# Performance work log

Hardware: AMD Instinct MI355X
Metric: run time of the kernel (lower is better)

Reference implementation:

```python
import jax, jax.numpy as jnp
import numpy as np

DIM = 2048
HEADS = 32
DIM_HEAD = 64
FF_INNER = DIM * 4
SCALE_BASE = 512
FUSED = HEADS * DIM_HEAD + DIM_HEAD + DIM_HEAD + FF_INNER * 2  # 18560


def setup_inputs() -> dict:
    key = jax.random.key(0)
    k1, k2, k3, k4 = jax.random.split(key, 4)
    b, n = 2, 2048
    x = jax.random.normal(k1, (b, n, DIM), dtype=jnp.float32)
    W_fused = jax.random.normal(k2, (FUSED, DIM), dtype=jnp.float32) * 0.02
    W_attn_out = jax.random.normal(k3, (DIM, HEADS * DIM_HEAD), dtype=jnp.float32) * 0.02
    W_ff_out = jax.random.normal(k4, (DIM, FF_INNER), dtype=jnp.float32) * 0.02
    gamma = jnp.ones((DIM,), dtype=jnp.float32)
    return {"x": x, "gamma": gamma, "W_fused": W_fused,
            "W_attn_out": W_attn_out, "W_ff_out": W_ff_out}


def _rotate_half(t):
    t1, t2 = jnp.split(t, 2, axis=-1)
    return jnp.concatenate((-t2, t1), axis=-1)


def _rotary(n, dtype):
    # xpos rotary embeddings: freqs [n, dim_head], scale [n, dim_head]
    inv_freq = 1.0 / (10000.0 ** (jnp.arange(0, DIM_HEAD, 2, dtype=jnp.float32) / DIM_HEAD))
    t = jnp.arange(n, dtype=jnp.float32)
    freqs = t[:, None] * inv_freq[None, :]
    freqs = jnp.concatenate((freqs, freqs), axis=-1)
    power = (t - n // 2) / SCALE_BASE
    scale_base_vec = (jnp.arange(0, DIM_HEAD, 2, dtype=jnp.float32) + 0.4 * DIM_HEAD) / (1.4 * DIM_HEAD)
    scale = scale_base_vec[None, :] ** power[:, None]
    scale = jnp.concatenate((scale, scale), axis=-1)
    return freqs.astype(dtype), scale.astype(dtype)


def _apply_rotary(pos, t, scale):
    return t * jnp.cos(pos) * scale + _rotate_half(t) * jnp.sin(pos) * scale


def reference(x, gamma, W_fused, W_attn_out, W_ff_out):
    b, n, d = x.shape
    # LayerNorm (beta fixed at zero)
    mu = jnp.mean(x, axis=-1, keepdims=True)
    var = jnp.mean((x - mu) ** 2, axis=-1, keepdims=True)
    xn = (x - mu) * jax.lax.rsqrt(var + 1e-5) * gamma

    # fused QKV + FF projection
    proj = jnp.einsum('bnd,fd->bnf', xn, W_fused)
    attn_inner = HEADS * DIM_HEAD
    q = proj[..., :attn_inner]
    k = proj[..., attn_inner:attn_inner + DIM_HEAD]
    v = proj[..., attn_inner + DIM_HEAD:attn_inner + 2 * DIM_HEAD]
    ff = proj[..., attn_inner + 2 * DIM_HEAD:]

    # multi-query attention with xpos rotary
    q = q.reshape(b, n, HEADS, DIM_HEAD).transpose(0, 2, 1, 3)  # b h n d
    q = q * (DIM_HEAD ** -0.5)
    pos, scale = _rotary(n, x.dtype)
    q = _apply_rotary(pos, q, scale)          # broadcasts over b,h
    k = _apply_rotary(pos, k, 1.0 / scale)    # k is [b, n, dim_head]

    sim = jnp.einsum('bhid,bjd->bhij', q, k)
    causal_mask = jnp.triu(jnp.ones((n, n), dtype=bool), k=1)
    sim = jnp.where(causal_mask, -jnp.finfo(sim.dtype).max, sim)
    attn = jax.nn.softmax(sim, axis=-1)
    out = jnp.einsum('bhij,bjd->bhid', attn, v)
    out = out.transpose(0, 2, 1, 3).reshape(b, n, attn_inner)
    attn_out = jnp.einsum('bnf,df->bnd', out, W_attn_out)

    # SwiGLU FF
    ff_x, gate = jnp.split(ff, 2, axis=-1)
    ff_hidden = jax.nn.silu(gate) * ff_x
    ff_out = jnp.einsum('bnf,df->bnd', ff_hidden, W_ff_out)

    return attn_out + ff_out
```

## Files before the change

### kernel.cpp

```cpp
#include <hip/hip_runtime.h>
#include <cstdint>
#include <cstddef>

typedef __bf16 bf16;
typedef float f32x4 __attribute__((ext_vector_type(4)));
typedef bf16  bf16x4 __attribute__((ext_vector_type(4)));
typedef bf16  bf16x8 __attribute__((ext_vector_type(8)));

#define DIMD   2048
#define HEADS  32
#define DH     64
#define FFI    8192
#define FUSEDN 18560
#define FUSEDP 18688
#define BB     2
#define NN     2048
#define MROWS  4096
#define K2     10240

__device__ __forceinline__ void gl_lds16(const void* g, void* l) {
  __builtin_amdgcn_global_load_lds(
      (__attribute__((address_space(1))) void*)const_cast<void*>(g),
      (__attribute__((address_space(3))) void*)l, 16, 0, 0);
}

template <int THREADS>
__device__ __forceinline__ void stage_i(const bf16* g, long ldk,
                                        bf16* region, int instr, int tid) {
  int row = instr * (THREADS / 8) + (tid >> 3);
  int cs  = (tid & 7) ^ (row & 7);
  gl_lds16(g + (size_t)row * ldk + cs * 8,
           region + (size_t)instr * (THREADS * 8) + (size_t)(tid & ~63) * 8);
}

struct SrcT { const bf16* g; long ldk; };

template <typename FA, typename FB>
__device__ __forceinline__ void gemm_2ph(FA fa, FB fb, const int NT,
    bf16* As, bf16* Bs, f32x4 (&acc)[4][4],
    const int tid, const int wrow, const int nbase, const int l15, const int h4)
{
  const char* aP[2]; const char* bP[2];
  const int arow = wrow + l15, brow = nbase + l15;
#pragma unroll
  for (int ks = 0; ks < 2; ks++) {
    aP[ks] = (const char*)As + arow * 128 + (((ks * 4 + h4) ^ (arow & 7)) * 16);
    bP[ks] = (const char*)Bs + brow * 128 + (((ks * 4 + h4) ^ (brow & 7)) * 16);
  }
  for (int t = 0; t < NT; ++t) {
    __syncthreads();
    {
      auto a = fa(t); auto b = fb(t);
#pragma unroll
      for (int q = 0; q < 4; q++) stage_i<256>(a.g, a.ldk, As, q, tid);
#pragma unroll
      for (int q = 0; q < 4; q++) stage_i<256>(b.g, b.ldk, Bs, q, tid);
    }
    __syncthreads();
#pragma unroll
    for (int ks = 0; ks < 2; ks++) {
      bf16x8 af[4], bfr[4];
#pragma unroll
      for (int m_ = 0; m_ < 4; m_++) af[m_]  = *(const bf16x8*)(aP[ks] + m_ * 2048);
#pragma unroll
      for (int n_ = 0; n_ < 4; n_++) bfr[n_] = *(const bf16x8*)(bP[ks] + n_ * 2048);
#pragma unroll
      for (int m_ = 0; m_ < 4; m_++)
#pragma unroll
        for (int n_ = 0; n_ < 4; n_++)
          acc[m_][n_] = __builtin_amdgcn_mfma_f32_16x16x32_bf16(af[m_], bfr[n_], acc[m_][n_], 0, 0, 0);
    }
  }
}

__global__ void k_cvt_perm(const float* __restrict__ s, bf16* __restrict__ d, long total8) {
  long stride = (long)gridDim.x * blockDim.x;
  for (long i = (long)blockIdx.x * blockDim.x + threadIdx.x; i < total8; i += stride) {
    long e = i << 3;
    int p = (int)(e >> 11);
    int c = (int)(e & 2047);
    int orig;
    if (p < 2176) orig = p;
    else {
      int q = p - 2176, g = q >> 6, o = q & 63;
      orig = (o < 32) ? (2176 + g * 32 + o) : (2176 + 8192 + g * 32 + (o - 32));
    }
    const float* src = s + (size_t)orig * 2048 + c;
    float4 v0 = *(const float4*)src;
    float4 v1 = *(const float4*)(src + 4);
    bf16x8 o8;
    o8[0]=(bf16)v0.x; o8[1]=(bf16)v0.y; o8[2]=(bf16)v0.z; o8[3]=(bf16)v0.w;
    o8[4]=(bf16)v1.x; o8[5]=(bf16)v1.y; o8[6]=(bf16)v1.z; o8[7]=(bf16)v1.w;
    *(bf16x8*)(d + e) = o8;
  }
}

__global__ void k_cvt_str8(const float* __restrict__ s, bf16* __restrict__ d,
                           long total8, int colshift, int dstride, int doff) {
  long stride = (long)gridDim.x * blockDim.x;
  for (long i = (long)blockIdx.x * blockDim.x + threadIdx.x; i < total8; i += stride) {
    long e = i << 3;
    long r = e >> colshift;
    int  c = (int)(e & ((1L << colshift) - 1));
    float4 v0 = *(const float4*)(s + e);
    float4 v1 = *(const float4*)(s + e + 4);
    bf16x8 o;
    o[0]=(bf16)v0.x; o[1]=(bf16)v0.y; o[2]=(bf16)v0.z; o[3]=(bf16)v0.w;
    o[4]=(bf16)v1.x; o[5]=(bf16)v1.y; o[6]=(bf16)v1.z; o[7]=(bf16)v1.w;
    *(bf16x8*)(d + r * (long)dstride + doff + c) = o;
  }
}

__global__ __launch_bounds__(256) void k_ln(const float* __restrict__ x,
                                            const float* __restrict__ g,
                                            bf16* __restrict__ xn) {
  int row = blockIdx.x, t = threadIdx.x;
  const float4* xr = (const float4*)(x + (size_t)row * DIMD);
  float4 a = xr[t*2], b = xr[t*2+1];
  float s  = a.x+a.y+a.z+a.w + b.x+b.y+b.z+b.w;
  float s2 = a.x*a.x+a.y*a.y+a.z*a.z+a.w*a.w + b.x*b.x+b.y*b.y+b.z*b.z+b.w*b.w;
  for (int o = 1; o < 64; o <<= 1) { s += __shfl_xor(s, o); s2 += __shfl_xor(s2, o); }
  __shared__ float rs[8];
  if ((t & 63) == 0) { rs[t>>6] = s; rs[4 + (t>>6)] = s2; }
  __syncthreads();
  s = rs[0]+rs[1]+rs[2]+rs[3]; s2 = rs[4]+rs[5]+rs[6]+rs[7];
  float mu = s * (1.f/DIMD);
  float var = s2 * (1.f/DIMD) - mu*mu;
  float rstd = rsqrtf(var + 1e-5f);
  const float4* gr = (const float4*)g;
  float4 g0 = gr[t*2], g1 = gr[t*2+1];
  bf16x8 o;
  o[0]=(bf16)((a.x-mu)*rstd*g0.x); o[1]=(bf16)((a.y-mu)*rstd*g0.y);
  o[2]=(bf16)((a.z-mu)*rstd*g0.z); o[3]=(bf16)((a.w-mu)*rstd*g0.w);
  o[4]=(bf16)((b.x-mu)*rstd*g1.x); o[5]=(bf16)((b.y-mu)*rstd*g1.y);
  o[6]=(bf16)((b.z-mu)*rstd*g1.z); o[7]=(bf16)((b.w-mu)*rstd*g1.w);
  *(bf16x8*)(xn + (size_t)row * DIMD + t*8) = o;
}

__global__ __launch_bounds__(256, 3) void k_gemm1(const bf16* __restrict__ xn,
                                                  const bf16* __restrict__ wf,
                                                  bf16* __restrict__ q_raw,
                                                  bf16* __restrict__ k_buf,
                                                  bf16* __restrict__ v_t,
                                                  bf16* __restrict__ ffh) {
  __shared__ bf16 As[128*64];
  __shared__ bf16 Bs[128*64];
  const int tid = threadIdx.x, w = tid >> 6, l = tid & 63;
  const int l15 = l & 15, h4 = l >> 4;
  const int wrow = (w >> 1) * 64, nbase = (w & 1) * 64;
  const int bid = blockIdx.x;
  const int bs = (bid & 7) * 584 + (bid >> 3);
  const int mt = bs / 146, nt = bs - mt * 146;
  const int m0 = mt * 128, f0 = nt * 128;

  f32x4 acc[4][4];
#pragma unroll
  for (int i = 0; i < 4; i++)
#pragma unroll
    for (int j = 0; j < 4; j++) acc[i][j] = (f32x4){0.f,0.f,0.f,0.f};

  auto fa = [&](int t) -> SrcT { return SrcT{ xn + (size_t)m0 * DIMD + t * 64, (long)DIMD }; };
  auto fb = [&](int t) -> SrcT { return SrcT{ wf + (size_t)f0 * DIMD + t * 64, (long)DIMD }; };
  gemm_2ph(fa, fb, DIMD / 64, As, Bs, acc, tid, wrow, nbase, l15, h4);

  if (nt < 17) {
#pragma unroll
    for (int m_ = 0; m_ < 4; m_++)
#pragma unroll
      for (int nf = 0; nf < 4; nf++) {
        int fcol = f0 + nbase + nf*16 + l15;
#pragma unroll
        for (int j = 0; j < 4; j++) {
          int m = m0 + wrow + m_*16 + h4*4 + j;
          bf16 bv = (bf16)acc[m_][nf][j];
          int b = m >> 11, n = m & 2047;
          if (fcol < 2048) {
            int hh = fcol >> 6, d = fcol & 63;
            q_raw[(((size_t)(b*HEADS + hh) * NN + n) << 6) + d] = bv;
          } else if (fcol < 2112) {
            k_buf[(((size_t)(b*NN + n)) << 6) + (fcol - 2048)] = bv;
          } else if (fcol < 2176) {
            v_t[(((size_t)(b*DH + (fcol - 2112))) << 11) + n] = bv;
          }
        }
      }
  } else {
    int base = f0 + nbase;
    if (base < FUSEDN) {
      int g = (base - 2176) >> 6;
#pragma unroll
      for (int m_ = 0; m_ < 4; m_++)
#pragma unroll
        for (int nf = 0; nf < 2; nf++) {
          int xc = g*32 + nf*16 + l15;
#pragma unroll
          for (int j = 0; j < 4; j++) {
            int m = m0 + wrow + m_*16 + h4*4 + j;
            float xv = acc[m_][nf][j];
            float gv = acc[m_][nf+2][j];
            float sv = gv * (1.f / (1.f + __expf(-gv)));
            ffh[((size_t)m << 13) + xc] = (bf16)(sv * xv);
          }
        }
    }
  }
}

__global__ __launch_bounds__(256, 3) void k_gemm2(const bf16* __restrict__ u_o,
                                                  const bf16* __restrict__ ffh,
                                                  const bf16* __restrict__ wcat,
                                                  float* __restrict__ out,
                                                  float* __restrict__ part) {
  __shared__ bf16 As[128*64];
  __shared__ bf16 Bs[128*64];
  const int tid = threadIdx.x, w = tid >> 6, l = tid & 63;
  const int l15 = l & 15, h4 = l >> 4;
  const int wrow = (w >> 1) * 64, nbase = (w & 1) * 64;
  const int bid = blockIdx.x;
  const int kk = bid >> 9;
  const int inner = bid & 511;
  const int bs = (inner & 7) * 64 + (inner >> 3);
  const int mt = bs >> 4, nt = bs & 15;
  const int m0 = mt * 128, f0 = nt * 128;
  const int T0 = kk * 80;

  f32x4 acc[4][4];
#pragma unroll
  for (int i = 0; i < 4; i++)
#pragma unroll
    for (int j = 0; j < 4; j++) acc[i][j] = (f32x4){0.f,0.f,0.f,0.f};

  auto fa = [&](int t) -> SrcT {
    int tt = t + T0;
    if (tt < 32) return SrcT{ u_o + (size_t)m0 * DIMD + tt * 64, (long)DIMD };
    return SrcT{ ffh + (size_t)m0 * FFI + (tt - 32) * 64, (long)FFI };
  };
  auto fb = [&](int t) -> SrcT { return SrcT{ wcat + (size_t)f0 * K2 + (t + T0) * 64, (long)K2 }; };
  gemm_2ph(fa, fb, 80, As, Bs, acc, tid, wrow, nbase, l15, h4);

  float* dst = kk ? part : out;
#pragma unroll
  for (int m_ = 0; m_ < 4; m_++)
#pragma unroll
    for (int nf = 0; nf < 4; nf++) {
      int fcol = f0 + nbase + nf*16 + l15;
#pragma unroll
      for (int j = 0; j < 4; j++) {
        int m = m0 + wrow + m_*16 + h4*4 + j;
        dst[(size_t)m * DIMD + fcol] = acc[m_][nf][j];
      }
    }
}

__global__ void k_addout(float* __restrict__ out, const float* __restrict__ part, long total4) {
  long stride = (long)gridDim.x * blockDim.x;
  for (long i = (long)blockIdx.x * blockDim.x + threadIdx.x; i < total4; i += stride) {
    long e = i << 2;
    float4 a = *(const float4*)(out + e);
    float4 b = *(const float4*)(part + e);
    float4 r; r.x = a.x + b.x; r.y = a.y + b.y; r.z = a.z + b.z; r.w = a.w + b.w;
    *(float4*)(out + e) = r;
  }
}

__global__ void k_rope(bf16* __restrict__ q_raw, bf16* __restrict__ k_buf) {
  const long QT = (long)BB*HEADS*NN*32;
  const long TOT = QT + (long)BB*NN*32;
  long gid = (long)blockIdx.x * blockDim.x + threadIdx.x;
  if (gid >= TOT) return;
  bool isq = gid < QT;
  long idx = isq ? gid : gid - QT;
  int  i = (int)(idx & 31);
  long row = idx >> 5;
  int  n = (int)(row & (NN - 1));
  bf16* base = (isq ? q_raw : k_buf) + row * DH;
  float t1 = (float)base[i];
  float t2 = (float)base[i + 32];
  float inv_freq = exp2f((float)i * -0.4152410118f);
  float th = (float)n * inv_freq;
  float sn, cs;
  __sincosf(th, &sn, &cs);
  float power = ((float)n - (float)(NN/2)) * (1.f/512.f);
  float sb = ((float)(2*i) + 25.6f) * (1.f/89.6f);
  float sc = exp2f((isq ? power : -power) * __log2f(sb));
  float mm = isq ? 0.125f : 1.0f;
  float o1 = (t1*cs - t2*sn) * sc * mm;
  float o2 = (t2*cs + t1*sn) * sc * mm;
  base[i]      = (bf16)o1;
  base[i + 32] = (bf16)o2;
}

__global__ __launch_bounds__(256) void k_attn(const bf16* __restrict__ qbuf,
                                              const bf16* __restrict__ kbuf,
                                              const bf16* __restrict__ vtb,
                                              bf16* __restrict__ uo) {
  __shared__ bf16 Qs[128*64];
  __shared__ bf16 Ks[32*64];
  __shared__ bf16 Vs[64*32];
  const int tid = threadIdx.x, w = tid >> 6, l = tid & 63;
  const int l15 = l & 15, h4 = l >> 4;
  const int bid = blockIdx.x;
  const int qt = 15 - (bid & 15);
  const int bh = bid >> 4;
  const int h = bh & (HEADS - 1), b = bh >> 5;
  const int q0 = qt * 128;
  const bf16* Qg = qbuf + ((size_t)(b*HEADS + h) * NN + q0) * DH;
  const bf16* Kg = kbuf + (size_t)b * NN * DH;
  const bf16* Vg = vtb + (size_t)b * DH * NN;

#pragma unroll
  for (int c = 0; c < 4; c++) {
    int chunk = c*256 + tid;
    int r = chunk >> 3, cc = chunk & 7;
    int col8 = (cc ^ (r & 7)) << 3;
    gl_lds16(Qg + (size_t)r*DH + col8, Qs + ((size_t)(chunk & ~63) << 3));
  }
  __syncthreads();

  const int wq0 = q0 + w*32;
  bf16x8 qfr[2][2];
#pragma unroll
  for (int qf = 0; qf < 2; qf++)
#pragma unroll
    for (int c = 0; c < 2; c++) {
      int row = w*32 + qf*16 + l15;
      int x = (64*c + 16*h4) ^ (16*(row & 7));
      qfr[qf][c] = *(const bf16x8*)((const char*)Qs + row*128 + x);
    }

  f32x4 zf = {0.f,0.f,0.f,0.f};
  f32x4 o_[2][4];
#pragma unroll
  for (int qf = 0; qf < 2; qf++)
#pragma unroll
    for (int nf = 0; nf < 4; nf++) o_[qf][nf] = zf;
  float mrun[2] = {-3e38f, -3e38f};
  float lrun[2] = {0.f, 0.f};

  const int nsteps = (q0 + 128) >> 5;
  for (int kt = 0; kt < nsteps; kt++) {
    const int kv0 = kt << 5;
    {
      int r = tid >> 3, cc = tid & 7;
      int col8 = (cc ^ (r & 7)) << 3;
      gl_lds16(Kg + (size_t)(kv0 + r)*DH + col8, Ks + ((size_t)(tid & ~63) << 3));
    }
    {
      int d = tid >> 2, cc = tid & 3;
      int col8 = (cc ^ (d & 3)) << 3;
      gl_lds16(Vg + (size_t)d*NN + kv0 + col8, Vs + ((size_t)(tid & ~63) << 3));
    }
    __syncthreads();
    if (kv0 <= wq0 + 31) {
      bf16x8 ka[2][2];
#pragma unroll
      for (int kvf = 0; kvf < 2; kvf++)
#pragma unroll
        for (int c = 0; c < 2; c++) {
          int r = kvf*16 + l15;
          int x = (64*c + 16*h4) ^ (16*(r & 7));
          ka[kvf][c] = *(const bf16x8*)((const char*)Ks + r*128 + x);
        }
      f32x4 st[2][2];
#pragma unroll
      for (int kvf = 0; kvf < 2; kvf++)
#pragma unroll
        for (int qf = 0; qf < 2; qf++) {
          f32x4 s = __builtin_amdgcn_mfma_f32_16x16x32_bf16(ka[kvf][0], qfr[qf][0], zf, 0, 0, 0);
          s = __builtin_amdgcn_mfma_f32_16x16x32_bf16(ka[kvf][1], qfr[qf][1], s, 0, 0, 0);
          st[kvf][qf] = s;
        }
      if (kv0 + 31 > wq0) {
#pragma unroll
        for (int kvf = 0; kvf < 2; kvf++)
#pragma unroll
          for (int j = 0; j < 4; j++) {
            int kvg = kv0 + kvf*16 + h4*4 + j;
#pragma unroll
            for (int qf = 0; qf < 2; qf++) {
              int qg = wq0 + qf*16 + l15;
              if (kvg > qg) st[kvf][qf][j] = -3e38f;
            }
          }
      }
      bf16x8 pa[2];
#pragma unroll
      for (int qf = 0; qf < 2; qf++) {
        float vmax = -3e38f;
#pragma unroll
        for (int kvf = 0; kvf < 2; kvf++)
#pragma unroll
          for (int j = 0; j < 4; j++) vmax = fmaxf(vmax, st[kvf][qf][j]);
        vmax = fmaxf(vmax, __shfl_xor(vmax, 16));
        vmax = fmaxf(vmax, __shfl_xor(vmax, 32));
        float mnew = fmaxf(mrun[qf], vmax);
        float corr = __expf(mrun[qf] - mnew);
        float ps = 0.f;
        float pv_[8];
#pragma unroll
        for (int kvf = 0; kvf < 2; kvf++)
#pragma unroll
          for (int j = 0; j < 4; j++) {
            float p = __expf(st[kvf][qf][j] - mnew);
            pv_[kvf*4 + j] = p; ps += p;
          }
        ps += __shfl_xor(ps, 16);
        ps += __shfl_xor(ps, 32);
        lrun[qf] = lrun[qf]*corr + ps;
        mrun[qf] = mnew;
        bf16x8 t;
#pragma unroll
        for (int i = 0; i < 8; i++) t[i] = (bf16)pv_[i];
        pa[qf] = t;
#pragma unroll
        for (int j = 0; j < 4; j++) {
          float cj = __shfl(corr, (l & 48) | (h4*4 + j), 64);
#pragma unroll
          for (int nf = 0; nf < 4; nf++) o_[qf][nf][j] *= cj;
        }
      }
#pragma unroll
      for (int nf = 0; nf < 4; nf++) {
        int d_ = nf*16 + l15;
        int swz = 16*(d_ & 3);
        const char* vrow = (const char*)Vs + d_*64;
        bf16x4 v0 = *(const bf16x4*)(vrow + ((8*h4) ^ swz));
        bf16x4 v1 = *(const bf16x4*)(vrow + ((8*h4 + 32) ^ swz));
        bf16x8 vb = __builtin_shufflevector(v0, v1, 0,1,2,3,4,5,6,7);
#pragma unroll
        for (int qf = 0; qf < 2; qf++)
          o_[qf][nf] = __builtin_amdgcn_mfma_f32_16x16x32_bf16(pa[qf], vb, o_[qf][nf], 0, 0, 0);
      }
    }
    __syncthreads();
  }
#pragma unroll
  for (int qf = 0; qf < 2; qf++) {
    float inv = 1.f / lrun[qf];
#pragma unroll
    for (int j = 0; j < 4; j++) {
      float ij = __shfl(inv, (l & 48) | (h4*4 + j), 64);
      int qg = wq0 + qf*16 + h4*4 + j;
      size_t rowoff = (size_t)(b*NN + qg) * DIMD + h*DH;
#pragma unroll
      for (int nf = 0; nf < 4; nf++)
        uo[rowoff + nf*16 + l15] = (bf16)(o_[qf][nf][j] * ij);
    }
  }
}

extern "C" void kernel_launch(void* const* d_in, const int* in_sizes, int n_in,
                              void* d_out, int out_size, void* d_ws, size_t ws_size,
                              hipStream_t stream) {
  const float* x     = (const float*)d_in[0];
  const float* gamma = (const float*)d_in[1];
  const float* Wf    = (const float*)d_in[2];
  const float* Wao   = (const float*)d_in[3];
  const float* Wff   = (const float*)d_in[4];
  float* out = (float*)d_out;
  char* ws = (char*)d_ws;

  size_t o = 0;
  bf16* wfb     = (bf16*)(ws + o); o += (size_t)FUSEDP * DIMD * 2;
  bf16* wcat    = wfb;
  bf16* xn      = (bf16*)(ws + o); o += (size_t)MROWS * DIMD * 2;
  bf16* q_raw   = (bf16*)(ws + o); o += (size_t)BB*HEADS*NN*DH * 2;
  bf16* k_buf   = (bf16*)(ws + o); o += (size_t)BB*NN*DH * 2;
  bf16* v_t     = (bf16*)(ws + o); o += (size_t)BB*DH*NN * 2;
  bf16* ffh     = (bf16*)(ws + o); o += (size_t)MROWS * FFI * 2;
  bf16* u_o     = (bf16*)(ws + o); o += (size_t)MROWS * DIMD * 2;
  float* part   = (float*)xn;

  k_cvt_perm<<<2048, 256, 0, stream>>>(Wf, wfb, (long)FUSEDN*DIMD/8);
  k_ln<<<MROWS, 256, 0, stream>>>(x, gamma, xn);
  k_gemm1<<<(FUSEDP/128)*(MROWS/128), 256, 0, stream>>>(xn, wfb, q_raw, k_buf, v_t, ffh);
  k_cvt_str8<<<512,  256, 0, stream>>>(Wao, wcat, (long)DIMD*DIMD/8, 11, K2, 0);
  k_cvt_str8<<<1024, 256, 0, stream>>>(Wff, wcat, (long)DIMD*FFI/8,  13, K2, DIMD);
  {
    long tot = (long)BB*HEADS*NN*32 + (long)BB*NN*32;
    k_rope<<<(int)((tot + 255) / 256), 256, 0, stream>>>(q_raw, k_buf);
  }
  k_attn<<<BB*HEADS*(NN/128), 256, 0, stream>>>(q_raw, k_buf, v_t, u_o);
  k_gemm2<<<2*(MROWS/128)*(DIMD/128), 256, 0, stream>>>(u_o, ffh, wcat, out, part);
  k_addout<<<2048, 256, 0, stream>>>(out, part, (long)MROWS*DIMD/4);
}
```

Baseline: 799.2 us.

## Fuse rotary embedding into GEMM1 epilogue, drop LDS staging in attention

Rotary position scaling for Q and K now happens in the first GEMM's epilogue, so the separate k_rope kernel and its extra read-write pass over Q/K go away. This relies on the fused column layout putting d and d+32 in the same thread's accumulators. The attention kernel now loads Q, K and V fragments straight from global memory instead of staging them through shared memory. That removes the block-wide barriers and lets each wave run only its own causal range, at the cost of uncoalesced, cache-dependent global loads. Both GEMMs also change tile rasterisation to iterate M fastest, for different L2 reuse.

```diff
diff --git a/kernel.cpp b/kernel.cpp
--- a/kernel.cpp
+++ b/kernel.cpp
@@ -150,7 +150,7 @@
   const int wrow = (w >> 1) * 64, nbase = (w & 1) * 64;
   const int bid = blockIdx.x;
   const int bs = (bid & 7) * 584 + (bid >> 3);
-  const int mt = bs / 146, nt = bs - mt * 146;
+  const int mt = bs & 31, nt = bs >> 5;
   const int m0 = mt * 128, f0 = nt * 128;
 
   f32x4 acc[4][4];
@@ -163,27 +163,74 @@
   auto fb = [&](int t) -> SrcT { return SrcT{ wf + (size_t)f0 * DIMD + t * 64, (long)DIMD }; };
   gemm_2ph(fa, fb, DIMD / 64, As, Bs, acc, tid, wrow, nbase, l15, h4);
 
-  if (nt < 17) {
+  if (nt < 16) {
+    const int hh = (f0 + nbase) >> 6;
+    float invf[2], lsb[2];
+#pragma unroll
+    for (int nf = 0; nf < 2; nf++) {
+      int i = nf*16 + l15;
+      invf[nf] = exp2f((float)i * -0.4152410118f);
+      lsb[nf]  = __log2f(((float)(2*i) + 25.6f) * (1.f/89.6f));
+    }
 #pragma unroll
     for (int m_ = 0; m_ < 4; m_++)
 #pragma unroll
-      for (int nf = 0; nf < 4; nf++) {
-        int fcol = f0 + nbase + nf*16 + l15;
+      for (int j = 0; j < 4; j++) {
+        int m = m0 + wrow + m_*16 + h4*4 + j;
+        int n = m & 2047, b = m >> 11;
+        float power = ((float)n - 1024.f) * (1.f/512.f);
+        bf16* qrow = q_raw + (((size_t)(b*HEADS + hh) * NN + n) << 6);
+#pragma unroll
+        for (int nf = 0; nf < 2; nf++) {
+          float t1 = acc[m_][nf][j], t2 = acc[m_][nf+2][j];
+          float sn, cs; __sincosf((float)n * invf[nf], &sn, &cs);
+          float sc = exp2f(power * lsb[nf]) * 0.125f;
+          int i = nf*16 + l15;
+          qrow[i]      = (bf16)((t1*cs - t2*sn) * sc);
+          qrow[i + 32] = (bf16)((t2*cs + t1*sn) * sc);
+        }
+      }
+  } else if (nt == 16) {
+    if (nbase == 0) {
+      float invf[2], lsb[2];
+#pragma unroll
+      for (int nf = 0; nf < 2; nf++) {
+        int i = nf*16 + l15;
+        invf[nf] = exp2f((float)i * -0.4152410118f);
+        lsb[nf]  = __log2f(((float)(2*i) + 25.6f) * (1.f/89.6f));
+      }
+#pragma unroll
+      for (int m_ = 0; m_ < 4; m_++)
 #pragma unroll
         for (int j = 0; j < 4; j++) {
           int m = m0 + wrow + m_*16 + h4*4 + j;
-          bf16 bv = (bf16)acc[m_][nf][j];
-          int b = m >> 11, n = m & 2047;
-          if (fcol < 2048) {
-            int hh = fcol >> 6, d = fcol & 63;
-            q_raw[(((size_t)(b*HEADS + hh) * NN + n) << 6) + d] = bv;
-          } else if (fcol < 2112) {
-            k_buf[(((size_t)(b*NN + n)) << 6) + (fcol - 2048)] = bv;
-          } else if (fcol < 2176) {
-            v_t[(((size_t)(b*DH + (fcol - 2112))) << 11) + n] = bv;
+          int n = m & 2047, b = m >> 11;
+          float power = ((float)n - 1024.f) * (1.f/512.f);
+          bf16* krow = k_buf + (((size_t)(b*NN + n)) << 6);
+#pragma unroll
+          for (int nf = 0; nf < 2; nf++) {
+            float t1 = acc[m_][nf][j], t2 = acc[m_][nf+2][j];
+            float sn, cs; __sincosf((float)n * invf[nf], &sn, &cs);
+            float sc = exp2f(-power * lsb[nf]);
+            int i = nf*16 + l15;
+            krow[i]      = (bf16)((t1*cs - t2*sn) * sc);
+            krow[i + 32] = (bf16)((t2*cs + t1*sn) * sc);
           }
         }
-      }
+    } else {
+#pragma unroll
+      for (int m_ = 0; m_ < 4; m_++)
+#pragma unroll
+        for (int nf = 0; nf < 4; nf++) {
+          int d = nf*16 + l15;
+#pragma unroll
+          for (int j = 0; j < 4; j++) {
+            int m = m0 + wrow + m_*16 + h4*4 + j;
+            int n = m & 2047, b = m >> 11;
+            v_t[(((size_t)(b*DH + d)) << 11) + n] = (bf16)acc[m_][nf][j];
+          }
+        }
+    }
   } else {
     int base = f0 + nbase;
     if (base < FUSEDN) {
@@ -220,7 +267,7 @@
   const int kk = bid >> 9;
   const int inner = bid & 511;
   const int bs = (inner & 7) * 64 + (inner >> 3);
-  const int mt = bs >> 4, nt = bs & 15;
+  const int mt = bs & 31, nt = bs >> 5;
   const int m0 = mt * 128, f0 = nt * 128;
   const int T0 = kk * 80;
 
@@ -263,70 +310,27 @@
   }
 }
 
-__global__ void k_rope(bf16* __restrict__ q_raw, bf16* __restrict__ k_buf) {
-  const long QT = (long)BB*HEADS*NN*32;
-  const long TOT = QT + (long)BB*NN*32;
-  long gid = (long)blockIdx.x * blockDim.x + threadIdx.x;
-  if (gid >= TOT) return;
-  bool isq = gid < QT;
-  long idx = isq ? gid : gid - QT;
-  int  i = (int)(idx & 31);
-  long row = idx >> 5;
-  int  n = (int)(row & (NN - 1));
-  bf16* base = (isq ? q_raw : k_buf) + row * DH;
-  float t1 = (float)base[i];
-  float t2 = (float)base[i + 32];
-  float inv_freq = exp2f((float)i * -0.4152410118f);
-  float th = (float)n * inv_freq;
-  float sn, cs;
-  __sincosf(th, &sn, &cs);
-  float power = ((float)n - (float)(NN/2)) * (1.f/512.f);
-  float sb = ((float)(2*i) + 25.6f) * (1.f/89.6f);
-  float sc = exp2f((isq ? power : -power) * __log2f(sb));
-  float mm = isq ? 0.125f : 1.0f;
-  float o1 = (t1*cs - t2*sn) * sc * mm;
-  float o2 = (t2*cs + t1*sn) * sc * mm;
-  base[i]      = (bf16)o1;
-  base[i + 32] = (bf16)o2;
-}
-
 __global__ __launch_bounds__(256) void k_attn(const bf16* __restrict__ qbuf,
                                               const bf16* __restrict__ kbuf,
                                               const bf16* __restrict__ vtb,
                                               bf16* __restrict__ uo) {
-  __shared__ bf16 Qs[128*64];
-  __shared__ bf16 Ks[32*64];
-  __shared__ bf16 Vs[64*32];
   const int tid = threadIdx.x, w = tid >> 6, l = tid & 63;
   const int l15 = l & 15, h4 = l >> 4;
   const int bid = blockIdx.x;
   const int qt = 15 - (bid & 15);
   const int bh = bid >> 4;
   const int h = bh & (HEADS - 1), b = bh >> 5;
-  const int q0 = qt * 128;
-  const bf16* Qg = qbuf + ((size_t)(b*HEADS + h) * NN + q0) * DH;
+  const int q0 = qt * 128, wq0 = q0 + w * 32;
+  const bf16* Qg = qbuf + (size_t)(b*HEADS + h) * NN * DH;
   const bf16* Kg = kbuf + (size_t)b * NN * DH;
   const bf16* Vg = vtb + (size_t)b * DH * NN;
 
-#pragma unroll
-  for (int c = 0; c < 4; c++) {
-    int chunk = c*256 + tid;
-    int r = chunk >> 3, cc = chunk & 7;
-    int col8 = (cc ^ (r & 7)) << 3;
-    gl_lds16(Qg + (size_t)r*DH + col8, Qs + ((size_t)(chunk & ~63) << 3));
-  }
-  __syncthreads();
-
-  const int wq0 = q0 + w*32;
   bf16x8 qfr[2][2];
 #pragma unroll
   for (int qf = 0; qf < 2; qf++)
 #pragma unroll
-    for (int c = 0; c < 2; c++) {
-      int row = w*32 + qf*16 + l15;
-      int x = (64*c + 16*h4) ^ (16*(row & 7));
-      qfr[qf][c] = *(const bf16x8*)((const char*)Qs + row*128 + x);
-    }
+    for (int c = 0; c < 2; c++)
+      qfr[qf][c] = *(const bf16x8*)(Qg + (size_t)(wq0 + qf*16 + l15) * DH + c*32 + h4*8);
 
   f32x4 zf = {0.f,0.f,0.f,0.f};
   f32x4 o_[2][4];
@@ -337,102 +341,84 @@
   float mrun[2] = {-3e38f, -3e38f};
   float lrun[2] = {0.f, 0.f};
 
-  const int nsteps = (q0 + 128) >> 5;
-  for (int kt = 0; kt < nsteps; kt++) {
+  const int nst = (wq0 >> 5) + 1;
+  for (int kt = 0; kt < nst; kt++) {
     const int kv0 = kt << 5;
-    {
-      int r = tid >> 3, cc = tid & 7;
-      int col8 = (cc ^ (r & 7)) << 3;
-      gl_lds16(Kg + (size_t)(kv0 + r)*DH + col8, Ks + ((size_t)(tid & ~63) << 3));
-    }
-    {
-      int d = tid >> 2, cc = tid & 3;
-      int col8 = (cc ^ (d & 3)) << 3;
-      gl_lds16(Vg + (size_t)d*NN + kv0 + col8, Vs + ((size_t)(tid & ~63) << 3));
-    }
-    __syncthreads();
-    if (kv0 <= wq0 + 31) {
-      bf16x8 ka[2][2];
+    bf16x8 ka[2][2];
+#pragma unroll
+    for (int kvf = 0; kvf < 2; kvf++)
+#pragma unroll
+      for (int c = 0; c < 2; c++)
+        ka[kvf][c] = *(const bf16x8*)(Kg + (size_t)(kv0 + kvf*16 + l15) * DH + c*32 + h4*8);
+    f32x4 st[2][2];
+#pragma unroll
+    for (int kvf = 0; kvf < 2; kvf++)
+#pragma unroll
+      for (int qf = 0; qf < 2; qf++) {
+        f32x4 s = __builtin_amdgcn_mfma_f32_16x16x32_bf16(ka[kvf][0], qfr[qf][0], zf, 0, 0, 0);
+        s = __builtin_amdgcn_mfma_f32_16x16x32_bf16(ka[kvf][1], qfr[qf][1], s, 0, 0, 0);
+        st[kvf][qf] = s;
+      }
+    if (kv0 + 31 > wq0) {
 #pragma unroll
       for (int kvf = 0; kvf < 2; kvf++)
 #pragma unroll
-        for (int c = 0; c < 2; c++) {
-          int r = kvf*16 + l15;
-          int x = (64*c + 16*h4) ^ (16*(r & 7));
-          ka[kvf][c] = *(const bf16x8*)((const char*)Ks + r*128 + x);
-        }
-      f32x4 st[2][2];
+        for (int j = 0; j < 4; j++) {
+          int kvg = kv0 + kvf*16 + h4*4 + j;
+#pragma unroll
+          for (int qf = 0; qf < 2; qf++) {
+            int qg = wq0 + qf*16 + l15;
+            if (kvg > qg) st[kvf][qf][j] = -3e38f;
+          }
+        }
+    }
+    bf16x8 pa[2];
+#pragma unroll
+    for (int qf = 0; qf < 2; qf++) {
+      float vmax = -3e38f;
 #pragma unroll
       for (int kvf = 0; kvf < 2; kvf++)
 #pragma unroll
-        for (int qf = 0; qf < 2; qf++) {
-          f32x4 s = __builtin_amdgcn_mfma_f32_16x16x32_bf16(ka[kvf][0], qfr[qf][0], zf, 0, 0, 0);
-          s = __builtin_amdgcn_mfma_f32_16x16x32_bf16(ka[kvf][1], qfr[qf][1], s, 0, 0, 0);
-          st[kvf][qf] = s;
-        }
-      if (kv0 + 31 > wq0) {
-#pragma unroll
-        for (int kvf = 0; kvf < 2; kvf++)
-#pragma unroll
-          for (int j = 0; j < 4; j++) {
-            int kvg = kv0 + kvf*16 + h4*4 + j;
-#pragma unroll
-            for (int qf = 0; qf < 2; qf++) {
-              int qg = wq0 + qf*16 + l15;
-              if (kvg > qg) st[kvf][qf][j] = -3e38f;
-            }
-          }
+        for (int j = 0; j < 4; j++) vmax = fmaxf(vmax, st[kvf][qf][j]);
+      vmax = fmaxf(vmax, __shfl_xor(vmax, 16));
+      vmax = fmaxf(vmax, __shfl_xor(vmax, 32));
+      float mnew = fmaxf(mrun[qf], vmax);
+      float corr = __expf(mrun[qf] - mnew);
+      float ps = 0.f;
+      float pv_[8];
+#pragma unroll
+      for (int kvf = 0; kvf < 2; kvf++)
+#pragma unroll
+        for (int j = 0; j < 4; j++) {
+          float p = __expf(st[kvf][qf][j] - mnew);
+          pv_[kvf*4 + j] = p; ps += p;
+        }
+      ps += __shfl_xor(ps, 16);
+      ps += __shfl_xor(ps, 32);
+      lrun[qf] = lrun[qf]*corr + ps;
+      mrun[qf] = mnew;
+      bf16x8 t;
+#pragma unroll
+      for (int i = 0; i < 8; i++) t[i] = (bf16)pv_[i];
+      pa[qf] = t;
+#pragma unroll
+      for (int j = 0; j < 4; j++) {
+        float cj = __shfl(corr, (l & 48) | (h4*4 + j), 64);
+#pragma unroll
+        for (int nf = 0; nf < 4; nf++) o_[qf][nf][j] *= cj;
       }
-      bf16x8 pa[2];
-#pragma unroll
-      for (int qf = 0; qf < 2; qf++) {
-        float vmax = -3e38f;
-#pragma unroll
-        for (int kvf = 0; kvf < 2; kvf++)
-#pragma unroll
-          for (int j = 0; j < 4; j++) vmax = fmaxf(vmax, st[kvf][qf][j]);
-        vmax = fmaxf(vmax, __shfl_xor(vmax, 16));
-        vmax = fmaxf(vmax, __shfl_xor(vmax, 32));
-        float mnew = fmaxf(mrun[qf], vmax);
-        float corr = __expf(mrun[qf] - mnew);
-        float ps = 0.f;
-        float pv_[8];
-#pragma unroll
-        for (int kvf = 0; kvf < 2; kvf++)
-#pragma unroll
-          for (int j = 0; j < 4; j++) {
-            float p = __expf(st[kvf][qf][j] - mnew);
-            pv_[kvf*4 + j] = p; ps += p;
-          }
-        ps += __shfl_xor(ps, 16);
-        ps += __shfl_xor(ps, 32);
-        lrun[qf] = lrun[qf]*corr + ps;
-        mrun[qf] = mnew;
-        bf16x8 t;
-#pragma unroll
-        for (int i = 0; i < 8; i++) t[i] = (bf16)pv_[i];
-        pa[qf] = t;
-#pragma unroll
-        for (int j = 0; j < 4; j++) {
-          float cj = __shfl(corr, (l & 48) | (h4*4 + j), 64);
-#pragma unroll
-          for (int nf = 0; nf < 4; nf++) o_[qf][nf][j] *= cj;
-        }
-      }
-#pragma unroll
-      for (int nf = 0; nf < 4; nf++) {
-        int d_ = nf*16 + l15;
-        int swz = 16*(d_ & 3);
-        const char* vrow = (const char*)Vs + d_*64;
-        bf16x4 v0 = *(const bf16x4*)(vrow + ((8*h4) ^ swz));
-        bf16x4 v1 = *(const bf16x4*)(vrow + ((8*h4 + 32) ^ swz));
-        bf16x8 vb = __builtin_shufflevector(v0, v1, 0,1,2,3,4,5,6,7);
-#pragma unroll
-        for (int qf = 0; qf < 2; qf++)
-          o_[qf][nf] = __builtin_amdgcn_mfma_f32_16x16x32_bf16(pa[qf], vb, o_[qf][nf], 0, 0, 0);
-      }
-    }
-    __syncthreads();
+    }
+#pragma unroll
+    for (int nf = 0; nf < 4; nf++) {
+      int d_ = nf*16 + l15;
+      const bf16* vr = Vg + (size_t)d_ * NN + kv0;
+      bf16x4 v0 = *(const bf16x4*)(vr + h4*4);
+      bf16x4 v1 = *(const bf16x4*)(vr + 16 + h4*4);
+      bf16x8 vb = __builtin_shufflevector(v0, v1, 0,1,2,3,4,5,6,7);
+#pragma unroll
+      for (int qf = 0; qf < 2; qf++)
+        o_[qf][nf] = __builtin_amdgcn_mfma_f32_16x16x32_bf16(pa[qf], vb, o_[qf][nf], 0, 0, 0);
+    }
   }
 #pragma unroll
   for (int qf = 0; qf < 2; qf++) {
@@ -476,10 +462,6 @@
   k_gemm1<<<(FUSEDP/128)*(MROWS/128), 256, 0, stream>>>(xn, wfb, q_raw, k_buf, v_t, ffh);
   k_cvt_str8<<<512,  256, 0, stream>>>(Wao, wcat, (long)DIMD*DIMD/8, 11, K2, 0);
   k_cvt_str8<<<1024, 256, 0, stream>>>(Wff, wcat, (long)DIMD*FFI/8,  13, K2, DIMD);
-  {
-    long tot = (long)BB*HEADS*NN*32 + (long)BB*NN*32;
-    k_rope<<<(int)((tot + 255) / 256), 256, 0, stream>>>(q_raw, k_buf);
-  }
   k_attn<<<BB*HEADS*(NN/128), 256, 0, stream>>>(q_raw, k_buf, v_t, u_o);
   k_gemm2<<<2*(MROWS/128)*(DIMD/128), 256, 0, stream>>>(u_o, ffh, wcat, out, part);
   k_addout<<<2048, 256, 0, stream>>>(out, part, (long)MROWS*DIMD/4);
```

New measurement: 950.2 us. 1.19x slower.
